# Performance work log

Measured on AMD Instinct MI355X. Metric: run time of the kernel, lower is better.

The kernel has to match this reference:

```python
import jax, jax.numpy as jnp
import numpy as np

C = 256
NH = 8
DH = C // NH
LN_EPS = 1e-5
COS_EPS = 1e-6


def _ln(x, w, b):
    m = x.mean(axis=-1, keepdims=True)
    v = ((x - m) ** 2).mean(axis=-1, keepdims=True)
    return (x - m) / jnp.sqrt(v + LN_EPS) * w + b


def _mha(q_in, kv_in, in_proj_w, in_proj_b, out_proj_w, out_proj_b):
    # q_in, kv_in: [P, S, C]. torch.nn.MultiheadAttention (batch_first).
    P, S, _ = q_in.shape
    q = q_in @ in_proj_w[:C].T + in_proj_b[:C]
    k = kv_in @ in_proj_w[C:2 * C].T + in_proj_b[C:2 * C]
    v = kv_in @ in_proj_w[2 * C:].T + in_proj_b[2 * C:]
    q = q.reshape(P, S, NH, DH)
    k = k.reshape(P, S, NH, DH)
    v = v.reshape(P, S, NH, DH)
    scores = jnp.einsum('pqhd,pkhd->phqk', q, k) / jnp.sqrt(jnp.asarray(DH, q.dtype))
    attn = jax.nn.softmax(scores, axis=-1)
    ctx = jnp.einsum('phqk,pkhd->pqhd', attn, v).reshape(P, S, C)
    return ctx @ out_proj_w.T + out_proj_b


def setup_inputs() -> dict:
    key = jax.random.key(0)
    ks = jax.random.split(key, 8)
    s = 0.02
    return {
        'z_sem': jax.random.normal(ks[0], (16, C, 32, 32), jnp.float32),
        'pair_indices': jnp.arange(16, dtype=jnp.int32).reshape(8, 2),
        'ln_w': jnp.ones((C,), jnp.float32),
        'ln_b': jnp.zeros((C,), jnp.float32),
        'in_proj_w': jax.random.normal(ks[1], (3 * C, C), jnp.float32) * s,
        'in_proj_b': jnp.zeros((3 * C,), jnp.float32),
        'out_proj_w': jax.random.normal(ks[2], (C, C), jnp.float32) * s,
        'out_proj_b': jnp.zeros((C,), jnp.float32),
        'res_scale': jnp.asarray(0.1, jnp.float32),
        'gate_scale': jnp.asarray(2.0, jnp.float32),
        'mlp_ln_w': jnp.ones((C,), jnp.float32),
        'mlp_ln_b': jnp.zeros((C,), jnp.float32),
        'mlp_w1': jax.random.normal(ks[3], (4 * C, C), jnp.float32) * s,
        'mlp_b1': jnp.zeros((4 * C,), jnp.float32),
        'mlp_w2': jax.random.normal(ks[4], (C, 4 * C), jnp.float32) * s,
        'mlp_b2': jnp.zeros((C,), jnp.float32),
    }


def reference(z_sem, pair_indices, ln_w, ln_b, in_proj_w, in_proj_b,
              out_proj_w, out_proj_b, res_scale, gate_scale,
              mlp_ln_w, mlp_ln_b, mlp_w1, mlp_b1, mlp_w2, mlp_b2):
    B, Cc, Hh, Ww = z_sem.shape
    S = Hh * Ww
    tokens = z_sem.reshape(B, Cc, S).transpose(0, 2, 1)  # [B, S, C]

    i_idx = pair_indices[:, 0]
    j_idx = pair_indices[:, 1]
    base_i = tokens[i_idx]  # [P, S, C]
    base_j = tokens[j_idx]

    q_i = _ln(base_i, ln_w, ln_b)
    q_j = _ln(base_j, ln_w, ln_b)

    cross_i = _mha(q_i, q_j, in_proj_w, in_proj_b, out_proj_w, out_proj_b)
    cross_j = _mha(q_j, q_i, in_proj_w, in_proj_b, out_proj_w, out_proj_b)

    # cosine similarity between mean-pooled normed tokens
    mi = q_i.mean(axis=1)  # [P, C]
    mj = q_j.mean(axis=1)
    ni = mi / jnp.maximum(jnp.linalg.norm(mi, axis=-1, keepdims=True), COS_EPS)
    nj = mj / jnp.maximum(jnp.linalg.norm(mj, axis=-1, keepdims=True), COS_EPS)
    sim = (ni * nj).sum(axis=-1)  # [P]
    gate = jax.nn.sigmoid(gate_scale * sim)  # [P]

    g = (res_scale * gate)[:, None, None]
    new_i = base_i + g * cross_i
    new_j = base_j + g * cross_j

    def _mlp(x):
        h = _ln(x, mlp_ln_w, mlp_ln_b)
        h = jax.nn.gelu(h @ mlp_w1.T + mlp_b1, approximate=False)
        return h @ mlp_w2.T + mlp_b2

    new_i = new_i + _mlp(new_i)
    new_j = new_j + _mlp(new_j)

    updated = tokens.at[i_idx].set(new_i).at[j_idx].set(new_j)
    shared = updated.transpose(0, 2, 1).reshape(B, Cc, Hh, Ww)
    return shared, gate, sim
```

## Files before the change

kernel.cpp:

```cpp
#include <hip/hip_runtime.h>
#include <hip/hip_bf16.h>

#define C_ 256
#define S_ 1024
#define NH_ 8
#define DH_ 32
#define NSIDE 16
#define MTOT (NSIDE * S_)

typedef __hip_bfloat16 bf16;
typedef short bf8_t __attribute__((ext_vector_type(8)));
typedef float f4_t __attribute__((ext_vector_type(4)));

#if __has_builtin(__builtin_amdgcn_exp2f)
#define QSCALE 0.25504167f
__device__ __forceinline__ float fastexp(float x) { return __builtin_amdgcn_exp2f(x); }
#else
#define QSCALE 0.17677669529663689f
__device__ __forceinline__ float fastexp(float x) { return __expf(x); }
#endif

__device__ __forceinline__ float b2f(bf16 x) { return __bfloat162float(x); }
__device__ __forceinline__ bf16 f2b(float x) { return __float2bfloat16(x); }
__device__ __forceinline__ unsigned short f2bu(float x) {
    bf16 h = f2b(x);
    return *reinterpret_cast<unsigned short*>(&h);
}
__device__ __forceinline__ unsigned pack_trunc(float a, float b) {
    return __builtin_amdgcn_perm(__float_as_uint(b), __float_as_uint(a), 0x07060302u);
}

__device__ __forceinline__ float block_sum(float v, float* red) {
#pragma unroll
    for (int off = 1; off < 64; off <<= 1) v += __shfl_xor(v, off);
    __syncthreads();
    if ((threadIdx.x & 63) == 0) red[threadIdx.x >> 6] = v;
    __syncthreads();
    float r = red[0] + red[1] + red[2] + red[3];
    __syncthreads();
    return r;
}

__device__ __forceinline__ void packone(const float* __restrict__ src, bf16* __restrict__ dst,
                                        int i, int kshift) {
    int n = i >> kshift, k = i & ((1 << kshift) - 1);
    size_t a = ((size_t)((n >> 4) * (1 << (kshift - 5)) + (k >> 5)) << 9) +
               (((k >> 3) & 3) << 7) + ((n & 15) << 3) + (k & 7);
    dst[a] = f2b(src[i]);
}

__global__ __launch_bounds__(256) void prep_kernel(
    const float* __restrict__ src, const int* __restrict__ pair,
    const float* __restrict__ w, const float* __restrict__ b,
    bf16* __restrict__ dst, float* __restrict__ partial,
    const float* __restrict__ wa, bf16* __restrict__ oa,
    const float* __restrict__ wb_, bf16* __restrict__ ob,
    const float* __restrict__ wc, bf16* __restrict__ oc,
    const float* __restrict__ wd, bf16* __restrict__ od) {
    int bid = blockIdx.x;
    if (bid >= 256) {
        int i = (bid - 256) * 256 + threadIdx.x;
        if (i < 196608) { packone(wa, oa, i, 8); return; }
        i -= 196608;
        if (i < 65536) { packone(wb_, ob, i, 8); return; }
        i -= 65536;
        if (i < 262144) { packone(wc, oc, i, 8); return; }
        i -= 262144;
        if (i < 262144) packone(wd, od, i, 10);
        return;
    }
    __shared__ float psum[4][64], psq[4][64], mean_s[64], rstd_s[64];
    __shared__ float wb[512];
    __shared__ __align__(16) short Ys[64][264];
    int sb = bid & 15, u = bid >> 4;
    int bi = pair[u];
    int tid = threadIdx.x;
    wb[tid] = w[tid];
    wb[256 + tid] = b[tid];
    int sl = tid & 63, cp = tid >> 6;
    int s = sb * 64 + sl;
    const float* zb = src + (size_t)bi * C_ * S_ + s;
    float sum = 0.f, sq = 0.f;
    for (int c = cp * 64; c < cp * 64 + 64; ++c) {
        float x = zb[(size_t)c * S_];
        sum += x;
        sq += x * x;
    }
    psum[cp][sl] = sum;
    psq[cp][sl] = sq;
    __syncthreads();
    if (tid < 64) {
        float sm = psum[0][tid] + psum[1][tid] + psum[2][tid] + psum[3][tid];
        float q2 = psq[0][tid] + psq[1][tid] + psq[2][tid] + psq[3][tid];
        float mean = sm * (1.0f / C_);
        float var = q2 * (1.0f / C_) - mean * mean;
        mean_s[tid] = mean;
        rstd_s[tid] = rsqrtf(var + 1e-5f);
    }
    __syncthreads();
    float mean = mean_s[sl], rstd = rstd_s[sl];
    int m = u * S_ + s;
    size_t tile8 = (size_t)(m >> 4) * 8;
    for (int c8 = 0; c8 < 64; c8 += 8) {
        int c = cp * 64 + c8;
        bf8_t pk;
#pragma unroll
        for (int j = 0; j < 8; ++j) {
            float x = zb[(size_t)(c + j) * S_];
            float y = (x - mean) * rstd * wb[c + j] + wb[256 + c + j];
            pk[j] = (short)f2bu(y);
        }
        *reinterpret_cast<bf8_t*>(&Ys[sl][c]) = pk;
        *reinterpret_cast<bf8_t*>(dst + ((tile8 + (c >> 5)) << 9) +
                                  (((c >> 3) & 3) << 7) + ((m & 15) << 3)) = pk;
    }
    __syncthreads();
    float csum = 0.f;
#pragma unroll 8
    for (int t = 0; t < 64; ++t)
        csum += b2f(*reinterpret_cast<const bf16*>(&Ys[t][tid]));
    partial[((size_t)u * 16 + sb) * C_ + tid] = csum;
}

__global__ __launch_bounds__(256) void gemm_qkv(
    const bf16* __restrict__ Apk, const bf16* __restrict__ Wpk, const float* __restrict__ bias,
    bf16* __restrict__ qpk, bf16* __restrict__ kpk, bf16* __restrict__ vpk,
    const float* __restrict__ partial, const float* __restrict__ gate_scale,
    float* __restrict__ gatef, float* __restrict__ out_gate, float* __restrict__ out_sim) {
    __shared__ float red[4];
    int tid = threadIdx.x;
    if (blockIdx.x == 768) {
        int c = tid;
        for (int p = 0; p < 8; ++p) {
            float mi = 0.f, mj = 0.f;
            for (int sy = 0; sy < 16; ++sy) {
                mi += partial[((size_t)(2 * p) * 16 + sy) * C_ + c];
                mj += partial[((size_t)(2 * p + 1) * 16 + sy) * C_ + c];
            }
            mi *= (1.f / S_);
            mj *= (1.f / S_);
            float ii = block_sum(mi * mi, red);
            float jj = block_sum(mj * mj, red);
            float ij = block_sum(mi * mj, red);
            if (c == 0) {
                float ni = fmaxf(sqrtf(ii), 1e-6f);
                float nj = fmaxf(sqrtf(jj), 1e-6f);
                float sim = ij / (ni * nj);
                float gate = 1.f / (1.f + expf(-gate_scale[0] * sim));
                gatef[p] = gate;
                out_gate[p] = gate;
                out_sim[p] = sim;
            }
        }
        return;
    }
    int wv = tid >> 6, lane = tid & 63;
    int ln15 = lane & 15, quad = lane >> 4;
    int idx = blockIdx.x * 4 + wv;
    int mt = idx / 12, nt = idx % 12;
    int m0 = mt * 64, n0 = nt * 64;

    f4_t acc[4][4];
#pragma unroll
    for (int i = 0; i < 4; ++i)
#pragma unroll
        for (int j = 0; j < 4; ++j) acc[i][j] = (f4_t)(0.0f);

    const bf16* Ab = Apk + ((size_t)mt << 14) + lane * 8;
    const bf16* Wb = Wpk + ((size_t)nt << 14) + lane * 8;

    bf8_t a0[4], w0[4], a1[4], w1[4];
#pragma unroll
    for (int i = 0; i < 4; ++i) {
        a0[i] = *reinterpret_cast<const bf8_t*>(Ab + ((size_t)(i * 8) << 9));
        w0[i] = *reinterpret_cast<const bf8_t*>(Wb + ((size_t)(i * 8) << 9));
    }
    for (int kch = 0; kch < 8; kch += 2) {
#pragma unroll
        for (int i = 0; i < 4; ++i) {
            a1[i] = *reinterpret_cast<const bf8_t*>(Ab + ((size_t)(i * 8 + kch + 1) << 9));
            w1[i] = *reinterpret_cast<const bf8_t*>(Wb + ((size_t)(i * 8 + kch + 1) << 9));
        }
#pragma unroll
        for (int i = 0; i < 4; ++i)
#pragma unroll
            for (int j = 0; j < 4; ++j)
                acc[i][j] = __builtin_amdgcn_mfma_f32_16x16x32_bf16(a0[i], w0[j], acc[i][j], 0, 0, 0);
        if (kch + 2 < 8) {
#pragma unroll
            for (int i = 0; i < 4; ++i) {
                a0[i] = *reinterpret_cast<const bf8_t*>(Ab + ((size_t)(i * 8 + kch + 2) << 9));
                w0[i] = *reinterpret_cast<const bf8_t*>(Wb + ((size_t)(i * 8 + kch + 2) << 9));
            }
        }
#pragma unroll
        for (int i = 0; i < 4; ++i)
#pragma unroll
            for (int j = 0; j < 4; ++j)
                acc[i][j] = __builtin_amdgcn_mfma_f32_16x16x32_bf16(a1[i], w1[j], acc[i][j], 0, 0, 0);
    }

#pragma unroll
    for (int i = 0; i < 4; ++i) {
#pragma unroll
        for (int j = 0; j < 4; ++j) {
            int coln = n0 + j * 16 + ln15;
            float bs = bias[coln];
            int row0 = m0 + i * 16 + quad * 4;
            int u = row0 >> 10, s0v = row0 & 1023;
            if (coln < 256) {
                int h = coln >> 5, d = coln & 31;
                bf16* qp = qpk + (((size_t)u * 8 + h) * 1024 + s0v) * 32 + d;
#pragma unroll
                for (int r = 0; r < 4; ++r)
                    qp[r * 32] = f2b((acc[i][j][r] + bs) * QSCALE);
            } else if (coln < 512) {
                int c = coln - 256, h = c >> 5, d = c & 31;
                bf16* kp = kpk + (((size_t)u * 8 + h) * 1024 + s0v) * 32 + d;
#pragma unroll
                for (int r = 0; r < 4; ++r)
                    kp[r * 32] = f2b(acc[i][j][r] + bs);
            } else {
                int c = coln - 512, h = c >> 5, d = c & 31;
                ushort4 pk;
#pragma unroll
                for (int r = 0; r < 4; ++r)
                    ((unsigned short*)&pk)[r] = f2bu(acc[i][j][r] + bs);
                *reinterpret_cast<ushort4*>(
                    vpk + ((((size_t)u * 8 + h) * 32 + (s0v >> 5)) * 32 + d) * 32 + (s0v & 31)) = pk;
            }
        }
    }
}

__global__ __launch_bounds__(256) void attn_mfma(const bf16* __restrict__ qpk,
                                                 const bf16* __restrict__ kpk,
                                                 const bf16* __restrict__ vpk,
                                                 bf16* __restrict__ ctx) {
    __shared__ __align__(16) short smem[4 * 2304];
    int tid = threadIdx.x;
    int wv = tid >> 6, lane = tid & 63;
    int ln15 = lane & 15, quad = lane >> 4;
    int bid = blockIdx.x;
    int g = bid >> 6, rem = bid & 63;
    int qb = rem >> 3, xcd = rem & 7;
    int uh = g * 8 + xcd;
    int u = uh >> 3, h = uh & 7, up = u ^ 1;
    int q0 = qb * 128 + wv * 32;
    short* PL = smem + wv * 2304;

    const bf16* Qb = qpk + (size_t)uh * 32768;
    const bf16* Kb = kpk + ((size_t)(up * 8 + h)) * 32768;
    const bf16* Vb = vpk + ((size_t)(up * 8 + h)) * 32768;

    bf8_t qf[2];
#pragma unroll
    for (int qt = 0; qt < 2; ++qt)
        qf[qt] = *reinterpret_cast<const bf8_t*>(Qb + (size_t)(q0 + qt * 16 + ln15) * 32 + quad * 8);

    bf8_t ones;
#pragma unroll
    for (int t = 0; t < 8; ++t) ones[t] = (short)0x3F80;

    const bf16* kp = Kb + ln15 * 32 + quad * 8;
    const bf16* vp = Vb + ln15 * 32 + quad * 8;
    short* plw = PL + ln15 * 72 + quad * 4;
    const short* plr = PL + ln15 * 72 + quad * 8;

    f4_t o[2][2];
#pragma unroll
    for (int i = 0; i < 2; ++i)
#pragma unroll
        for (int j = 0; j < 2; ++j) o[i][j] = (f4_t)(0.0f);
    f4_t lacc[2];
    lacc[0] = (f4_t)(0.0f);
    lacc[1] = (f4_t)(0.0f);
    f4_t zf = (f4_t)(0.0f);

    bf8_t kfA[4], vtA[2][2], kfB[4], vtB[2][2];
#pragma unroll
    for (int t = 0; t < 4; ++t)
        kfA[t] = *reinterpret_cast<const bf8_t*>(kp + (size_t)(t * 16) * 32);
#pragma unroll
    for (int kc = 0; kc < 2; ++kc)
#pragma unroll
        for (int dh = 0; dh < 2; ++dh)
            vtA[kc][dh] = *reinterpret_cast<const bf8_t*>(vp + (size_t)kc * 1024 + dh * 512);

    auto step = [&](bf8_t (&kfC)[4], bf8_t (&vtC)[2][2],
                    bf8_t (&kfN)[4], bf8_t (&vtN)[2][2], int itn) {
        f4_t st[4][2];
#pragma unroll
        for (int kh = 0; kh < 4; ++kh)
#pragma unroll
            for (int qt = 0; qt < 2; ++qt)
                st[kh][qt] = __builtin_amdgcn_mfma_f32_16x16x32_bf16(kfC[kh], qf[qt], zf, 0, 0, 0);
        if (itn < 16) {
            int k0n = itn * 64;
#pragma unroll
            for (int t = 0; t < 4; ++t)
                kfN[t] = *reinterpret_cast<const bf8_t*>(kp + (size_t)(k0n + t * 16) * 32);
#pragma unroll
            for (int kc = 0; kc < 2; ++kc)
#pragma unroll
                for (int dh = 0; dh < 2; ++dh)
                    vtN[kc][dh] = *reinterpret_cast<const bf8_t*>(vp + (size_t)(itn * 2 + kc) * 1024 + dh * 512);
        }
#pragma unroll
        for (int qt = 0; qt < 2; ++qt) {
#pragma unroll
            for (int kh = 0; kh < 4; ++kh) {
                float e0 = fastexp(st[kh][qt][0]);
                float e1 = fastexp(st[kh][qt][1]);
                float e2 = fastexp(st[kh][qt][2]);
                float e3 = fastexp(st[kh][qt][3]);
                uint2 pk;
                pk.x = pack_trunc(e0, e1);
                pk.y = pack_trunc(e2, e3);
                *reinterpret_cast<uint2*>(plw + qt * 1152 + kh * 16) = pk;
            }
        }
#pragma unroll
        for (int qt = 0; qt < 2; ++qt) {
#pragma unroll
            for (int kc = 0; kc < 2; ++kc) {
                bf8_t pf = *reinterpret_cast<const bf8_t*>(plr + qt * 1152 + kc * 32);
                o[0][qt] = __builtin_amdgcn_mfma_f32_16x16x32_bf16(vtC[kc][0], pf, o[0][qt], 0, 0, 0);
                o[1][qt] = __builtin_amdgcn_mfma_f32_16x16x32_bf16(vtC[kc][1], pf, o[1][qt], 0, 0, 0);
                lacc[qt] = __builtin_amdgcn_mfma_f32_16x16x32_bf16(ones, pf, lacc[qt], 0, 0, 0);
            }
        }
    };

    for (int it = 0; it < 16; it += 2) {
        step(kfA, vtA, kfB, vtB, it + 1);
        step(kfB, vtB, kfA, vtA, it + 2);
    }

#pragma unroll
    for (int qt = 0; qt < 2; ++qt) {
        float inv = 1.f / lacc[qt][0];
        size_t base = ((size_t)(u * S_ + q0 + qt * 16 + ln15)) * C_ + h * DH_;
#pragma unroll
        for (int dh = 0; dh < 2; ++dh) {
            ushort4 pk;
            pk.x = f2bu(o[dh][qt][0] * inv);
            pk.y = f2bu(o[dh][qt][1] * inv);
            pk.z = f2bu(o[dh][qt][2] * inv);
            pk.w = f2bu(o[dh][qt][3] * inv);
            *reinterpret_cast<ushort4*>(ctx + base + dh * 16 + quad * 4) = pk;
        }
    }
}

__global__ __launch_bounds__(512) void fused_tail(
    const bf16* __restrict__ ctx, const bf16* __restrict__ wout,
    const float* __restrict__ bout, const float* __restrict__ z,
    const int* __restrict__ pair, const float* __restrict__ gatef,
    const float* __restrict__ res_scale,
    const float* __restrict__ lnw, const float* __restrict__ lnb,
    const bf16* __restrict__ w1b, const float* __restrict__ b1,
    const bf16* __restrict__ w2b, const float* __restrict__ b2,
    float* __restrict__ outp) {
    __shared__ __align__(16) short Xs[32][264];
    __shared__ __align__(16) short CHs[32][264];
    __shared__ float ssum[8][32], ssq[8][32], smean[32], srstd[32];

    int tid = threadIdx.x;
    int wv = tid >> 6, lane = tid & 63;
    int ln15 = lane & 15, quad = lane >> 4;
    int u = blockIdx.x >> 5;
    int s0 = (blockIdx.x & 31) * 32;
    int bi = pair[u];
    float g = res_scale[0] * gatef[u >> 1];
    int c0 = wv * 32;

    {
        int row = tid >> 4, col = (tid & 15) * 16;
        const bf16* src = ctx + ((size_t)(u * S_ + s0 + row)) * 256 + col;
        *reinterpret_cast<bf8_t*>(&CHs[row][col]) = *reinterpret_cast<const bf8_t*>(src);
        *reinterpret_cast<bf8_t*>(&CHs[row][col + 8]) = *reinterpret_cast<const bf8_t*>(src + 8);
    }
    __syncthreads();

    f4_t yacc[2][2];
#pragma unroll
    for (int i = 0; i < 2; ++i)
#pragma unroll
        for (int j = 0; j < 2; ++j) yacc[i][j] = (f4_t)(0.0f);
    {
        const bf16* Wb = wout + (((size_t)(wv * 2) * 8) << 9) + lane * 8;
#pragma unroll
        for (int kch = 0; kch < 8; ++kch) {
            bf8_t wf[2], xf[2];
#pragma unroll
            for (int i = 0; i < 2; ++i)
                wf[i] = *reinterpret_cast<const bf8_t*>(Wb + ((size_t)(i * 8 + kch) << 9));
#pragma unroll
            for (int j = 0; j < 2; ++j)
                xf[j] = *reinterpret_cast<const bf8_t*>(&CHs[j * 16 + ln15][kch * 32 + quad * 8]);
#pragma unroll
            for (int i = 0; i < 2; ++i)
#pragma unroll
                for (int j = 0; j < 2; ++j)
                    yacc[i][j] = __builtin_amdgcn_mfma_f32_16x16x32_bf16(wf[i], xf[j], yacc[i][j], 0, 0, 0);
        }
    }
    float psum[2] = {0.f, 0.f}, psq[2] = {0.f, 0.f};
#pragma unroll
    for (int i = 0; i < 2; ++i) {
#pragma unroll
        for (int r = 0; r < 4; ++r) {
            int c = c0 + i * 16 + quad * 4 + r;
            float bs = bout[c];
            const float* zr = z + ((size_t)bi * C_ + c) * S_ + s0;
#pragma unroll
            for (int j = 0; j < 2; ++j) {
                int sl = j * 16 + ln15;
                float y = zr[sl] + g * (yacc[i][j][r] + bs);
                yacc[i][j][r] = y;
                psum[j] += y;
                psq[j] += y * y;
            }
        }
    }
#pragma unroll
    for (int j = 0; j < 2; ++j) {
        psum[j] += __shfl_xor(psum[j], 16);
        psum[j] += __shfl_xor(psum[j], 32);
        psq[j] += __shfl_xor(psq[j], 16);
        psq[j] += __shfl_xor(psq[j], 32);
    }
    if (quad == 0) {
#pragma unroll
        for (int j = 0; j < 2; ++j) {
            ssum[wv][j * 16 + ln15] = psum[j];
            ssq[wv][j * 16 + ln15] = psq[j];
        }
    }
    __syncthreads();
    if (tid < 32) {
        float sm = 0.f, q2 = 0.f;
#pragma unroll
        for (int w = 0; w < 8; ++w) {
            sm += ssum[w][tid];
            q2 += ssq[w][tid];
        }
        float mean = sm * (1.0f / C_);
        float var = q2 * (1.0f / C_) - mean * mean;
        smean[tid] = mean;
        srstd[tid] = rsqrtf(var + 1e-5f);
    }
    __syncthreads();
#pragma unroll
    for (int j = 0; j < 2; ++j) {
        int sl = j * 16 + ln15;
        float mean = smean[sl], rstd = srstd[sl];
#pragma unroll
        for (int i = 0; i < 2; ++i) {
            ushort4 pk;
#pragma unroll
            for (int r = 0; r < 4; ++r) {
                int c = c0 + i * 16 + quad * 4 + r;
                float xv = (yacc[i][j][r] - mean) * rstd * lnw[c] + lnb[c];
                ((unsigned short*)&pk)[r] = f2bu(xv);
            }
            *reinterpret_cast<ushort4*>(&Xs[sl][c0 + i * 16 + quad * 4]) = pk;
        }
    }
    __syncthreads();

    f4_t acc2[2][2];
#pragma unroll
    for (int i = 0; i < 2; ++i)
#pragma unroll
        for (int j = 0; j < 2; ++j) acc2[i][j] = (f4_t)(0.0f);

    for (int pass = 0; pass < 4; ++pass) {
        f4_t hacc[2][2];
#pragma unroll
        for (int i = 0; i < 2; ++i)
#pragma unroll
            for (int j = 0; j < 2; ++j) hacc[i][j] = (f4_t)(0.0f);
        {
            const bf16* W1p = w1b + (((size_t)(pass * 16 + wv * 2) * 8) << 9) + lane * 8;
#pragma unroll
            for (int kch = 0; kch < 8; ++kch) {
                bf8_t wf[2], xf[2];
#pragma unroll
                for (int i = 0; i < 2; ++i)
                    wf[i] = *reinterpret_cast<const bf8_t*>(W1p + ((size_t)(i * 8 + kch) << 9));
#pragma unroll
                for (int j = 0; j < 2; ++j)
                    xf[j] = *reinterpret_cast<const bf8_t*>(&Xs[j * 16 + ln15][kch * 32 + quad * 8]);
#pragma unroll
                for (int i = 0; i < 2; ++i)
#pragma unroll
                    for (int j = 0; j < 2; ++j)
                        hacc[i][j] = __builtin_amdgcn_mfma_f32_16x16x32_bf16(wf[i], xf[j], hacc[i][j], 0, 0, 0);
            }
        }
#pragma unroll
        for (int j = 0; j < 2; ++j) {
#pragma unroll
            for (int i = 0; i < 2; ++i) {
                ushort4 pk;
#pragma unroll
                for (int r = 0; r < 4; ++r) {
                    int hg = pass * 256 + c0 + i * 16 + quad * 4 + r;
                    float v = hacc[i][j][r] + b1[hg];
                    float ge = 0.5f * v * (1.f + erff(v * 0.70710678118f));
                    ((unsigned short*)&pk)[r] = f2bu(ge);
                }
                *reinterpret_cast<ushort4*>(&CHs[j * 16 + ln15][c0 + i * 16 + quad * 4]) = pk;
            }
        }
        __syncthreads();
        {
            const bf16* W2p = w2b + (((size_t)(wv * 2) * 32 + pass * 8) << 9) + lane * 8;
#pragma unroll
            for (int kch = 0; kch < 8; ++kch) {
                bf8_t wf[2], hf[2];
#pragma unroll
                for (int i = 0; i < 2; ++i)
                    wf[i] = *reinterpret_cast<const bf8_t*>(W2p + ((size_t)(i * 32 + kch) << 9));
#pragma unroll
                for (int j = 0; j < 2; ++j)
                    hf[j] = *reinterpret_cast<const bf8_t*>(&CHs[j * 16 + ln15][kch * 32 + quad * 8]);
#pragma unroll
                for (int i = 0; i < 2; ++i)
#pragma unroll
                    for (int j = 0; j < 2; ++j)
                        acc2[i][j] = __builtin_amdgcn_mfma_f32_16x16x32_bf16(wf[i], hf[j], acc2[i][j], 0, 0, 0);
            }
        }
        __syncthreads();
    }

#pragma unroll
    for (int i = 0; i < 2; ++i) {
#pragma unroll
        for (int r = 0; r < 4; ++r) {
            int c = c0 + i * 16 + quad * 4 + r;
            float bs = b2[c];
            float* orow = outp + ((size_t)bi * C_ + c) * S_ + s0;
#pragma unroll
            for (int j = 0; j < 2; ++j)
                orow[j * 16 + ln15] = yacc[i][j][r] + acc2[i][j][r] + bs;
        }
    }
}

extern "C" void kernel_launch(void* const* d_in, const int* in_sizes, int n_in,
                              void* d_out, int out_size, void* d_ws, size_t ws_size,
                              hipStream_t stream) {
    const float* z = (const float*)d_in[0];
    const int* pair = (const int*)d_in[1];
    const float* ln_w = (const float*)d_in[2];
    const float* ln_b = (const float*)d_in[3];
    const float* in_proj_w = (const float*)d_in[4];
    const float* in_proj_b = (const float*)d_in[5];
    const float* out_proj_w = (const float*)d_in[6];
    const float* out_proj_b = (const float*)d_in[7];
    const float* res_scale = (const float*)d_in[8];
    const float* gate_scale = (const float*)d_in[9];
    const float* mlp_ln_w = (const float*)d_in[10];
    const float* mlp_ln_b = (const float*)d_in[11];
    const float* mlp_w1 = (const float*)d_in[12];
    const float* mlp_b1 = (const float*)d_in[13];
    const float* mlp_w2 = (const float*)d_in[14];
    const float* mlp_b2 = (const float*)d_in[15];
    float* out = (float*)d_out;

    char* ws = (char*)d_ws;
    bf16* qln = (bf16*)(ws);
    bf16* qpk = (bf16*)(ws + 8388608);
    bf16* kpk = (bf16*)(ws + 16777216);
    bf16* vpk = (bf16*)(ws + 25165824);
    bf16* ctx = (bf16*)(ws + 33554432);
    bf16* wqkv = (bf16*)(ws + 41943040);
    bf16* wout = (bf16*)(ws + 41943040 + 393216);
    bf16* w1b = (bf16*)(ws + 41943040 + 524288);
    bf16* w2b = (bf16*)(ws + 41943040 + 1048576);
    float* partial = (float*)(ws + 50331648);
    float* gatef = (float*)(ws + 50331648 + 262144);

    prep_kernel<<<3328, 256, 0, stream>>>(z, pair, ln_w, ln_b, qln, partial,
                                          in_proj_w, wqkv, out_proj_w, wout,
                                          mlp_w1, w1b, mlp_w2, w2b);
    gemm_qkv<<<769, 256, 0, stream>>>(qln, wqkv, in_proj_b, qpk, kpk, vpk,
                                      partial, gate_scale, gatef,
                                      out + 4194304, out + 4194312);
    attn_mfma<<<1024, 256, 0, stream>>>(qpk, kpk, vpk, ctx);
    fused_tail<<<512, 512, 0, stream>>>(ctx, wout, out_proj_b, z, pair, gatef, res_scale,
                                        mlp_ln_w, mlp_ln_b, w1b, mlp_b1, w2b, mlp_b2, out);
}
```

Before: 217.2 us.

## Double queries per attention wave to reuse K/V fragments across more rows

Each wave now processes 64 query rows instead of 32, so every K/V fragment loaded from global memory is reused across four query tiles, and the grid is halved to 512 blocks. The score-exp-pack loop is split per query tile to limit live score registers, LDS for the P tile doubles, and launch bounds request 2 blocks per CU. The goal is less K/V load traffic per unit of work, at the cost of more registers and LDS per block and fewer blocks to hide latency.

Result: faster. 204.9 us, median of 2 (-5.7%).

```diff
diff --git a/kernel.cpp b/kernel.cpp
--- a/kernel.cpp
+++ b/kernel.cpp
@@ -233,29 +233,29 @@
     }
 }
 
-__global__ __launch_bounds__(256) void attn_mfma(const bf16* __restrict__ qpk,
-                                                 const bf16* __restrict__ kpk,
-                                                 const bf16* __restrict__ vpk,
-                                                 bf16* __restrict__ ctx) {
-    __shared__ __align__(16) short smem[4 * 2304];
+__global__ __launch_bounds__(256, 2) void attn_mfma(const bf16* __restrict__ qpk,
+                                                    const bf16* __restrict__ kpk,
+                                                    const bf16* __restrict__ vpk,
+                                                    bf16* __restrict__ ctx) {
+    __shared__ __align__(16) short smem[4 * 4608];
     int tid = threadIdx.x;
     int wv = tid >> 6, lane = tid & 63;
     int ln15 = lane & 15, quad = lane >> 4;
     int bid = blockIdx.x;
-    int g = bid >> 6, rem = bid & 63;
+    int g = bid >> 5, rem = bid & 31;
     int qb = rem >> 3, xcd = rem & 7;
     int uh = g * 8 + xcd;
     int u = uh >> 3, h = uh & 7, up = u ^ 1;
-    int q0 = qb * 128 + wv * 32;
-    short* PL = smem + wv * 2304;
+    int q0 = qb * 256 + wv * 64;
+    short* PL = smem + wv * 4608;
 
     const bf16* Qb = qpk + (size_t)uh * 32768;
     const bf16* Kb = kpk + ((size_t)(up * 8 + h)) * 32768;
     const bf16* Vb = vpk + ((size_t)(up * 8 + h)) * 32768;
 
-    bf8_t qf[2];
-#pragma unroll
-    for (int qt = 0; qt < 2; ++qt)
+    bf8_t qf[4];
+#pragma unroll
+    for (int qt = 0; qt < 4; ++qt)
         qf[qt] = *reinterpret_cast<const bf8_t*>(Qb + (size_t)(q0 + qt * 16 + ln15) * 32 + quad * 8);
 
     bf8_t ones;
@@ -267,14 +267,14 @@
     short* plw = PL + ln15 * 72 + quad * 4;
     const short* plr = PL + ln15 * 72 + quad * 8;
 
-    f4_t o[2][2];
+    f4_t o[2][4];
 #pragma unroll
     for (int i = 0; i < 2; ++i)
 #pragma unroll
-        for (int j = 0; j < 2; ++j) o[i][j] = (f4_t)(0.0f);
-    f4_t lacc[2];
-    lacc[0] = (f4_t)(0.0f);
-    lacc[1] = (f4_t)(0.0f);
+        for (int j = 0; j < 4; ++j) o[i][j] = (f4_t)(0.0f);
+    f4_t lacc[4];
+#pragma unroll
+    for (int j = 0; j < 4; ++j) lacc[j] = (f4_t)(0.0f);
     f4_t zf = (f4_t)(0.0f);
 
     bf8_t kfA[4], vtA[2][2], kfB[4], vtB[2][2];
@@ -289,31 +289,46 @@
 
     auto step = [&](bf8_t (&kfC)[4], bf8_t (&vtC)[2][2],
                     bf8_t (&kfN)[4], bf8_t (&vtN)[2][2], int itn) {
-        f4_t st[4][2];
-#pragma unroll
-        for (int kh = 0; kh < 4; ++kh)
-#pragma unroll
-            for (int qt = 0; qt < 2; ++qt)
-                st[kh][qt] = __builtin_amdgcn_mfma_f32_16x16x32_bf16(kfC[kh], qf[qt], zf, 0, 0, 0);
-        if (itn < 16) {
-            int k0n = itn * 64;
-#pragma unroll
-            for (int t = 0; t < 4; ++t)
-                kfN[t] = *reinterpret_cast<const bf8_t*>(kp + (size_t)(k0n + t * 16) * 32);
-#pragma unroll
-            for (int kc = 0; kc < 2; ++kc)
-#pragma unroll
-                for (int dh = 0; dh < 2; ++dh)
-                    vtN[kc][dh] = *reinterpret_cast<const bf8_t*>(vp + (size_t)(itn * 2 + kc) * 1024 + dh * 512);
-        }
-#pragma unroll
-        for (int qt = 0; qt < 2; ++qt) {
+        {
+            f4_t st[4];
+#pragma unroll
+            for (int kh = 0; kh < 4; ++kh)
+                st[kh] = __builtin_amdgcn_mfma_f32_16x16x32_bf16(kfC[kh], qf[0], zf, 0, 0, 0);
+            if (itn < 16) {
+                int k0n = itn * 64;
+#pragma unroll
+                for (int t = 0; t < 4; ++t)
+                    kfN[t] = *reinterpret_cast<const bf8_t*>(kp + (size_t)(k0n + t * 16) * 32);
+#pragma unroll
+                for (int kc = 0; kc < 2; ++kc)
+#pragma unroll
+                    for (int dh = 0; dh < 2; ++dh)
+                        vtN[kc][dh] = *reinterpret_cast<const bf8_t*>(vp + (size_t)(itn * 2 + kc) * 1024 + dh * 512);
+            }
 #pragma unroll
             for (int kh = 0; kh < 4; ++kh) {
-                float e0 = fastexp(st[kh][qt][0]);
-                float e1 = fastexp(st[kh][qt][1]);
-                float e2 = fastexp(st[kh][qt][2]);
-                float e3 = fastexp(st[kh][qt][3]);
+                float e0 = fastexp(st[kh][0]);
+                float e1 = fastexp(st[kh][1]);
+                float e2 = fastexp(st[kh][2]);
+                float e3 = fastexp(st[kh][3]);
+                uint2 pk;
+                pk.x = pack_trunc(e0, e1);
+                pk.y = pack_trunc(e2, e3);
+                *reinterpret_cast<uint2*>(plw + kh * 16) = pk;
+            }
+        }
+#pragma unroll
+        for (int qt = 1; qt < 4; ++qt) {
+            f4_t st[4];
+#pragma unroll
+            for (int kh = 0; kh < 4; ++kh)
+                st[kh] = __builtin_amdgcn_mfma_f32_16x16x32_bf16(kfC[kh], qf[qt], zf, 0, 0, 0);
+#pragma unroll
+            for (int kh = 0; kh < 4; ++kh) {
+                float e0 = fastexp(st[kh][0]);
+                float e1 = fastexp(st[kh][1]);
+                float e2 = fastexp(st[kh][2]);
+                float e3 = fastexp(st[kh][3]);
                 uint2 pk;
                 pk.x = pack_trunc(e0, e1);
                 pk.y = pack_trunc(e2, e3);
@@ -321,7 +336,7 @@
             }
         }
 #pragma unroll
-        for (int qt = 0; qt < 2; ++qt) {
+        for (int qt = 0; qt < 4; ++qt) {
 #pragma unroll
             for (int kc = 0; kc < 2; ++kc) {
                 bf8_t pf = *reinterpret_cast<const bf8_t*>(plr + qt * 1152 + kc * 32);
@@ -338,7 +353,7 @@
     }
 
 #pragma unroll
-    for (int qt = 0; qt < 2; ++qt) {
+    for (int qt = 0; qt < 4; ++qt) {
         float inv = 1.f / lacc[qt][0];
         size_t base = ((size_t)(u * S_ + q0 + qt * 16 + ln15)) * C_ + h * DH_;
 #pragma unroll
@@ -591,7 +606,7 @@
     gemm_qkv<<<769, 256, 0, stream>>>(qln, wqkv, in_proj_b, qpk, kpk, vpk,
                                       partial, gate_scale, gatef,
                                       out + 4194304, out + 4194312);
-    attn_mfma<<<1024, 256, 0, stream>>>(qpk, kpk, vpk, ctx);
+    attn_mfma<<<512, 256, 0, stream>>>(qpk, kpk, vpk, ctx);
     fused_tail<<<512, 512, 0, stream>>>(ctx, wout, out_proj_b, z, pair, gatef, res_scale,
                                         mlp_ln_w, mlp_ln_b, w1b, mlp_b1, w2b, mlp_b2, out);
 }
```
